# Kernel tuning notes

Measured on AMD Instinct MI355X. Metric: run time of the kernel, lower is better.

The kernel has to match this reference:

```python
import jax, jax.numpy as jnp
import numpy as np

N = 4096
IN_DIM, HID, OUT_DIM = 512, 256, 64
PROP_STEP = 10
LAM_HAT = 0.9
SCAD_A = 3.7
EPS = 1e-8


def setup_inputs() -> dict:
    key = jax.random.key(0)
    kA, kF, k1, k2 = jax.random.split(key, 4)
    # sparse symmetric 0/1 adjacency, zero diagonal (add_loops adds I later)
    u = jax.random.uniform(kA, (N, N), dtype=jnp.float32)
    A = (u < 0.005).astype(jnp.float32)
    A = jnp.maximum(A, A.T)
    A = A * (1.0 - jnp.eye(N, dtype=jnp.float32))
    F = jax.random.normal(kF, (N, IN_DIM), dtype=jnp.float32)
    W1 = jax.random.normal(k1, (IN_DIM, HID), dtype=jnp.float32) / np.sqrt(IN_DIM)
    b1 = jnp.zeros((HID,), dtype=jnp.float32)
    W2 = jax.random.normal(k2, (HID, OUT_DIM), dtype=jnp.float32) / np.sqrt(HID)
    b2 = jnp.zeros((OUT_DIM,), dtype=jnp.float32)
    raw_gamma = jnp.zeros((PROP_STEP,), dtype=jnp.float32)
    return {"A": A, "F": F, "W1": W1, "b1": b1, "W2": W2, "b2": b2,
            "raw_gamma": raw_gamma}


def reference(A, F, W1, b1, W2, b2, raw_gamma):
    lam = 1.0 / LAM_HAT - 1.0
    a = SCAD_A
    # MLP (dropout inactive at inference)
    F0 = jax.nn.relu(F @ W1 + b1) @ W2 + b2            # [N, out_dim]
    eye = jnp.eye(A.shape[0], dtype=A.dtype)
    A = A + eye                                        # add_loops
    D = A.sum(-1)                                      # [N]
    D_sq = jnp.sqrt(D)[:, None]                        # [N, 1]
    A_tilde = A / D_sq / D_sq.T                        # sym_norm: D^-1/2 A D^-1/2
    gammas = jax.nn.sigmoid(raw_gamma) * 2.0           # per-layer gamma in (0, 2)

    def step(Fc, gamma_k):
        Fn = Fc / D_sq
        nrm = jnp.linalg.norm(Fn, axis=-1, keepdims=True)
        Fu = Fn / jnp.maximum(nrm, 1e-12)
        # cosine distance in [0, 2]; detached as in torch (.detach())
        y = jax.lax.stop_gradient(1.0 - Fu @ Fu.T)     # [N, N]
        lam_k = jnp.maximum(gamma_k / a, EPS)
        t = a * lam_k
        safe_y = jnp.where(y <= 0.0, 1.0, y)
        w_mid = (t - y) / ((a - 1.0) * safe_y)
        # SCAD weight: 1 for y<=lam_k, linear decay on [lam_k, a*lam_k], 0 beyond
        W = jnp.where(y <= lam_k, 1.0, jnp.where(y <= t, w_mid, 0.0))
        W = W * (1.0 - eye)
        W = jnp.where(jnp.isnan(W), 1.0, W)
        Q_hat = ((W * A).sum(-1) / D + lam)[:, None]   # [N, 1]
        F_new = (W * A_tilde) @ Fc / Q_hat + lam * F0 / Q_hat
        return F_new, None

    F_out, _ = jax.lax.scan(step, F0, gammas)
    return F_out
```

## Files before the change

kernel.cpp:

```cpp
#include <hip/hip_runtime.h>
#include <hip/hip_bf16.h>

#define N_NODES 4096
#define IN_DIM  512
#define HID_DIM 256
#define OUT_DIM 64
#define PROP_STEP 10
#define MAX_DEG 128
#define GEMM_BLOCKS 256
#define SCAN_BLOCKS 256
#define LAM_CONST (1.0f/0.9f - 1.0f)
#define SCAD_A 3.7f

__device__ __forceinline__ ushort f2bf(float f) {
    unsigned u = __float_as_uint(f);
    unsigned r = (u + 0x7FFFu + ((u >> 16) & 1u)) >> 16;
    return (ushort)r;
}
__device__ __forceinline__ unsigned pack2(float lo, float hi) {
    return (unsigned)f2bf(lo) | ((unsigned)f2bf(hi) << 16);
}
__device__ __forceinline__ float bflo(unsigned u) { return __uint_as_float(u << 16); }
__device__ __forceinline__ float bfhi(unsigned u) { return __uint_as_float(u & 0xFFFF0000u); }

__global__ __launch_bounds__(512) void build_all(
    const float* __restrict__ A, const float* __restrict__ F,
    const float* __restrict__ W1, const float* __restrict__ b1,
    const float* __restrict__ W2, const float* __restrict__ b2,
    float* __restrict__ F0,
    int* __restrict__ ell, int* __restrict__ deg,
    float* __restrict__ invD, float* __restrict__ invDsq)
{
    if (blockIdx.x < GEMM_BLOCKS) {
        __shared__ float sFt[16][20];
        __shared__ float sW[16][272];
        __shared__ float sH[16][260];
        int t  = threadIdx.x;
        int m0 = blockIdx.x * 16;
        int tm = (t & 7) * 2;
        int tn = (t >> 3) * 4;
        int fr = t >> 4, fk = t & 15;
        int wr = t >> 6, wc = (t & 63) * 4;
        float a00 = 0.f, a01 = 0.f, a02 = 0.f, a03 = 0.f;
        float a10 = 0.f, a11 = 0.f, a12 = 0.f, a13 = 0.f;
        for (int kc = 0; kc < IN_DIM; kc += 16) {
            float fv = 0.0f;
            if (t < 256) fv = F[(size_t)(m0 + fr) * IN_DIM + kc + fk];
            float4 w0 = *(const float4*)(W1 + (size_t)(kc + wr)     * HID_DIM + wc);
            float4 w1 = *(const float4*)(W1 + (size_t)(kc + 8 + wr) * HID_DIM + wc);
            __syncthreads();
            if (t < 256) sFt[fk][fr] = fv;
            *(float4*)&sW[wr][wc]     = w0;
            *(float4*)&sW[8 + wr][wc] = w1;
            __syncthreads();
#pragma unroll
            for (int k = 0; k < 16; k++) {
                float2 a = *(const float2*)&sFt[k][tm];
                float4 b = *(const float4*)&sW[k][tn];
                a00 += a.x * b.x; a01 += a.x * b.y; a02 += a.x * b.z; a03 += a.x * b.w;
                a10 += a.y * b.x; a11 += a.y * b.y; a12 += a.y * b.z; a13 += a.y * b.w;
            }
        }
        float4 bb = *(const float4*)(b1 + tn);
        *(float4*)&sH[tm][tn] = make_float4(
            fmaxf(a00 + bb.x, 0.f), fmaxf(a01 + bb.y, 0.f),
            fmaxf(a02 + bb.z, 0.f), fmaxf(a03 + bb.w, 0.f));
        *(float4*)&sH[tm + 1][tn] = make_float4(
            fmaxf(a10 + bb.x, 0.f), fmaxf(a11 + bb.y, 0.f),
            fmaxf(a12 + bb.z, 0.f), fmaxf(a13 + bb.w, 0.f));
        __syncthreads();
        int r2 = t >> 5;
        int c2 = (t & 31) * 2;
        float accA = b2[c2], accB = b2[c2 + 1];
        float (*sW2c)[68] = (float(*)[68])sW;
        for (int kc = 0; kc < HID_DIM; kc += 64) {
            __syncthreads();
            for (int i = t; i < 1024; i += 512) {
                int kk = i >> 4, cc = (i & 15) * 4;
                *(float4*)&sW2c[kk][cc] =
                    *(const float4*)(W2 + (size_t)(kc + kk) * OUT_DIM + cc);
            }
            __syncthreads();
#pragma unroll 8
            for (int k = 0; k < 64; k++) {
                float  hb = sH[r2][kc + k];
                float2 w2 = *(const float2*)&sW2c[k][c2];
                accA += hb * w2.x; accB += hb * w2.y;
            }
        }
        *(float2*)(F0 + (size_t)(m0 + r2) * OUT_DIM + c2) = make_float2(accA, accB);
    } else {
        int sb   = blockIdx.x - GEMM_BLOCKS;
        int lane = threadIdx.x & 63;
        int wid  = threadIdx.x >> 6;
        int w    = sb * 8 + wid;
        for (int rr = 0; rr < 2; rr++) {
            int row = w * 2 + rr;
            const float* Arow = A + (size_t)row * N_NODES;
            float4 ch[16];
#pragma unroll
            for (int c = 0; c < 16; c++)
                ch[c] = *(const float4*)(Arow + c * 256 + lane * 4);
            int* rdst = ell + (size_t)row * MAX_DEG;
            unsigned cnt = 0;
#pragma unroll
            for (int c = 0; c < 16; c++) {
                float4 v = ch[c];
                int colbase = c * 256 + lane * 4;
#pragma unroll
                for (int q = 0; q < 4; q++) {
                    float vv = (q == 0) ? v.x : (q == 1) ? v.y : (q == 2) ? v.z : v.w;
                    bool nz = (vv != 0.0f);
                    unsigned long long m = __ballot(nz);
                    unsigned rank = __builtin_amdgcn_mbcnt_hi(
                        (unsigned)(m >> 32),
                        __builtin_amdgcn_mbcnt_lo((unsigned)m, 0u));
                    unsigned pos = cnt + rank;
                    if (nz && pos < MAX_DEG) rdst[pos] = colbase + q;
                    cnt += (unsigned)__popcll(m);
                }
            }
            int c  = (cnt > MAX_DEG) ? MAX_DEG : (int)cnt;
            int pad = (c + 15) & ~15;
            if (pad > MAX_DEG) pad = MAX_DEG;
            if (lane >= c && lane < pad) rdst[lane] = row;
            int l2 = lane + 64;
            if (l2 >= c && l2 < pad) rdst[l2] = row;
            if (lane == 0) {
                deg[row] = c;
                float d = (float)(cnt + 1);
                invD[row] = 1.0f / d;
                invDsq[row] = rsqrtf(d);
            }
        }
    }
}

__global__ __launch_bounds__(256, 4) void propagate_f0(
    const float* __restrict__ F0,
    const int* __restrict__ ell, const int* __restrict__ deg,
    const float* __restrict__ invD, const float* __restrict__ invDsq,
    const float* __restrict__ raw_gamma,
    unsigned* __restrict__ Pout, float* __restrict__ nrmOut)
{
    int lane = threadIdx.x & 63;
    int wid  = threadIdx.x >> 6;
    int r    = __builtin_amdgcn_readfirstlane(blockIdx.x * 4 + wid);
    int g    = lane >> 3;
    int sl   = lane & 7;
    const float inv_am1 = 1.0f / (SCAD_A - 1.0f);

    float gamma = 2.0f / (1.0f + expf(-raw_gamma[0]));
    float lam_k = fmaxf(gamma / SCAD_A, 1e-8f);
    float tt    = SCAD_A * lam_k;

    int dg = deg[r];
    int pad = (dg + 15) & ~15;
    int npair = pad >> 4;
    const int* nb = ell + (size_t)r * MAX_DEG;
    int ed0 = (lane < pad)      ? nb[lane]      : r;
    int ed1 = (64 + lane < pad) ? nb[64 + lane] : r;

    float iDs = invDsq[r];
    const float4* f04 = (const float4*)(F0 + (size_t)r * OUT_DIM + sl * 8);
    float4 fa = f04[0], fb = f04[1];
    float f0v[8] = { fa.x, fa.y, fa.z, fa.w, fb.x, fb.y, fb.z, fb.w };
    float ui[8];
    float ssr = 0.0f;
#pragma unroll
    for (int q = 0; q < 8; q++) { ui[q] = f0v[q] * iDs; ssr += ui[q] * ui[q]; }
    ssr += __shfl_xor(ssr, 1, 64);
    ssr += __shfl_xor(ssr, 2, 64);
    ssr += __shfl_xor(ssr, 4, 64);
    float inv_nr = 1.0f / fmaxf(sqrtf(ssr), 1e-12f);
#pragma unroll
    for (int q = 0; q < 8; q++) ui[q] *= inv_nr;

    float acc[8] = {};
    float qsum = 0.0f;
    for (int it = 0; it < npair; ++it) {
        int e0 = it * 16 + g, e1 = e0 + 8;
        int src = (it < 4) ? ed0 : ed1;
        int j0 = __shfl(src, e0 & 63, 64);
        int j1 = __shfl(src, e1 & 63, 64);
        const float4* p0 = (const float4*)(F0 + (size_t)j0 * OUT_DIM + sl * 8);
        const float4* p1 = (const float4*)(F0 + (size_t)j1 * OUT_DIM + sl * 8);
        float4 x0 = p0[0], x1 = p0[1];
        float4 y0 = p1[0], y1 = p1[1];
        float d0 = invDsq[j0], d1 = invDsq[j1];
        float v0[8] = { x0.x*d0, x0.y*d0, x0.z*d0, x0.w*d0, x1.x*d0, x1.y*d0, x1.z*d0, x1.w*d0 };
        float v1[8] = { y0.x*d1, y0.y*d1, y0.z*d1, y0.w*d1, y1.x*d1, y1.y*d1, y1.z*d1, y1.w*d1 };
        float pa = 0.f, pb = 0.f, s0 = 0.f, s1 = 0.f;
#pragma unroll
        for (int q = 0; q < 8; q++) {
            pa += ui[q] * v0[q]; s0 += v0[q] * v0[q];
            pb += ui[q] * v1[q]; s1 += v1[q] * v1[q];
        }
        pa += __shfl_xor(pa, 1, 64); pb += __shfl_xor(pb, 1, 64);
        s0 += __shfl_xor(s0, 1, 64); s1 += __shfl_xor(s1, 1, 64);
        pa += __shfl_xor(pa, 2, 64); pb += __shfl_xor(pb, 2, 64);
        s0 += __shfl_xor(s0, 2, 64); s1 += __shfl_xor(s1, 2, 64);
        pa += __shfl_xor(pa, 4, 64); pb += __shfl_xor(pb, 4, 64);
        s0 += __shfl_xor(s0, 4, 64); s1 += __shfl_xor(s1, 4, 64);
        float n0 = fmaxf(sqrtf(s0), 1e-12f);
        float n1 = fmaxf(sqrtf(s1), 1e-12f);
        float ya = 1.0f - pa / n0, yb = 1.0f - pb / n1;
        float wa = (ya <= lam_k) ? 1.0f : ((ya <= tt) ? (tt - ya) * inv_am1 / ya : 0.0f);
        float wb = (yb <= lam_k) ? 1.0f : ((yb <= tt) ? (tt - yb) * inv_am1 / yb : 0.0f);
        if (e0 >= dg) wa = 0.0f;
        if (e1 >= dg) wb = 0.0f;
        qsum += wa + wb;
#pragma unroll
        for (int q = 0; q < 8; q++) acc[q] += wa * v0[q] + wb * v1[q];
    }

#pragma unroll
    for (int off = 8; off <= 32; off <<= 1) {
#pragma unroll
        for (int q = 0; q < 8; q++) acc[q] += __shfl_xor(acc[q], off, 64);
        qsum += __shfl_xor(qsum, off, 64);
    }

    float Qh  = qsum * invD[r] + LAM_CONST;
    float rQh = 1.0f / Qh;
    float res[8], fn[8];
    float ssq = 0.0f;
#pragma unroll
    for (int q = 0; q < 8; q++) {
        res[q] = (acc[q] * iDs + LAM_CONST * f0v[q]) * rQh;
        fn[q]  = res[q] * iDs;
        ssq   += fn[q] * fn[q];
    }
    ssq += __shfl_xor(ssq, 1, 64);
    ssq += __shfl_xor(ssq, 2, 64);
    ssq += __shfl_xor(ssq, 4, 64);
    float nrm = fmaxf(sqrtf(ssq), 1e-12f);
    float inv_n = 1.0f / nrm;
    if (lane < 8) {
        uint4 fuPk;
        fuPk.x = pack2(fn[0] * inv_n, fn[1] * inv_n);
        fuPk.y = pack2(fn[2] * inv_n, fn[3] * inv_n);
        fuPk.z = pack2(fn[4] * inv_n, fn[5] * inv_n);
        fuPk.w = pack2(fn[6] * inv_n, fn[7] * inv_n);
        *(uint4*)(Pout + (size_t)r * 32 + sl * 4) = fuPk;
    }
    if (lane == 0) nrmOut[r] = nrm;
}

__global__ __launch_bounds__(256, 4) void propagate(
    const unsigned* __restrict__ Pin, const float* __restrict__ nrmIn,
    const float* __restrict__ F0,
    const int* __restrict__ ell, const int* __restrict__ deg,
    const float* __restrict__ invD, const float* __restrict__ invDsq,
    const float* __restrict__ raw_gamma, int step,
    unsigned* __restrict__ Pout, float* __restrict__ nrmOut,
    float* __restrict__ FcOut, int writeNext, int writeOut)
{
    int lane = threadIdx.x & 63;
    int wid  = threadIdx.x >> 6;
    int r    = __builtin_amdgcn_readfirstlane(blockIdx.x * 4 + wid);
    int g    = lane >> 3;
    int sl   = lane & 7;
    const float inv_am1 = 1.0f / (SCAD_A - 1.0f);

    float gamma = 2.0f / (1.0f + expf(-raw_gamma[step]));
    float lam_k = fmaxf(gamma / SCAD_A, 1e-8f);
    float tt    = SCAD_A * lam_k;

    int dg = deg[r];
    int pad = (dg + 15) & ~15;
    int npair = pad >> 4;
    const int* nb = ell + (size_t)r * MAX_DEG;
    int ed0 = (lane < pad)      ? nb[lane]      : r;
    int ed1 = (64 + lane < pad) ? nb[64 + lane] : r;

    uint4 up = *(const uint4*)(Pin + (size_t)r * 32 + sl * 4);
    float ui[8] = { bflo(up.x), bfhi(up.x), bflo(up.y), bfhi(up.y),
                    bflo(up.z), bfhi(up.z), bflo(up.w), bfhi(up.w) };

    float acc[8] = {};
    float qsum = 0.0f;

    auto eidx = [&](int it_, int& J0, int& J1) {
        int e0_ = it_ * 16 + g;
        int src = (it_ < 4) ? ed0 : ed1;
        J0 = __shfl(src, e0_ & 63, 64);
        J1 = __shfl(src, (e0_ + 8) & 63, 64);
    };
    auto body = [&](int it_, uint4 U0, uint4 U1, float NR0, float NR1) {
        float pa = ui[0] * bflo(U0.x) + ui[1] * bfhi(U0.x) + ui[2] * bflo(U0.y) + ui[3] * bfhi(U0.y)
                 + ui[4] * bflo(U0.z) + ui[5] * bfhi(U0.z) + ui[6] * bflo(U0.w) + ui[7] * bfhi(U0.w);
        float pb = ui[0] * bflo(U1.x) + ui[1] * bfhi(U1.x) + ui[2] * bflo(U1.y) + ui[3] * bfhi(U1.y)
                 + ui[4] * bflo(U1.z) + ui[5] * bfhi(U1.z) + ui[6] * bflo(U1.w) + ui[7] * bfhi(U1.w);
        pa += __shfl_xor(pa, 1, 64); pb += __shfl_xor(pb, 1, 64);
        pa += __shfl_xor(pa, 2, 64); pb += __shfl_xor(pb, 2, 64);
        pa += __shfl_xor(pa, 4, 64); pb += __shfl_xor(pb, 4, 64);
        float ya = 1.0f - pa, yb = 1.0f - pb;
        float wa = (ya <= lam_k) ? 1.0f : ((ya <= tt) ? (tt - ya) * inv_am1 / ya : 0.0f);
        float wb = (yb <= lam_k) ? 1.0f : ((yb <= tt) ? (tt - yb) * inv_am1 / yb : 0.0f);
        int e0_ = it_ * 16 + g;
        if (e0_ >= dg)     wa = 0.0f;
        if (e0_ + 8 >= dg) wb = 0.0f;
        qsum += wa + wb;
        float wsa = wa * NR0;
        float wsb = wb * NR1;
        acc[0] += wsa * bflo(U0.x) + wsb * bflo(U1.x);
        acc[1] += wsa * bfhi(U0.x) + wsb * bfhi(U1.x);
        acc[2] += wsa * bflo(U0.y) + wsb * bflo(U1.y);
        acc[3] += wsa * bfhi(U0.y) + wsb * bfhi(U1.y);
        acc[4] += wsa * bflo(U0.z) + wsb * bflo(U1.z);
        acc[5] += wsa * bfhi(U0.z) + wsb * bfhi(U1.z);
        acc[6] += wsa * bflo(U0.w) + wsb * bflo(U1.w);
        acc[7] += wsa * bfhi(U0.w) + wsb * bfhi(U1.w);
    };

    if (npair > 0) {
        uint4 uA0, uA1, uB0, uB1;
        float nA0, nA1, nB0, nB1;
        int j0, j1;
        eidx(0, j0, j1);
        uA0 = *(const uint4*)(Pin + (size_t)j0 * 32 + sl * 4);
        uA1 = *(const uint4*)(Pin + (size_t)j1 * 32 + sl * 4);
        nA0 = nrmIn[j0]; nA1 = nrmIn[j1];
        int it = 0;
        while (true) {
            if (it + 1 < npair) {
                eidx(it + 1, j0, j1);
                uB0 = *(const uint4*)(Pin + (size_t)j0 * 32 + sl * 4);
                uB1 = *(const uint4*)(Pin + (size_t)j1 * 32 + sl * 4);
                nB0 = nrmIn[j0]; nB1 = nrmIn[j1];
            }
            body(it, uA0, uA1, nA0, nA1);
            ++it; if (it >= npair) break;
            if (it + 1 < npair) {
                eidx(it + 1, j0, j1);
                uA0 = *(const uint4*)(Pin + (size_t)j0 * 32 + sl * 4);
                uA1 = *(const uint4*)(Pin + (size_t)j1 * 32 + sl * 4);
                nA0 = nrmIn[j0]; nA1 = nrmIn[j1];
            }
            body(it, uB0, uB1, nB0, nB1);
            ++it; if (it >= npair) break;
        }
    }

#pragma unroll
    for (int off = 8; off <= 32; off <<= 1) {
#pragma unroll
        for (int q = 0; q < 8; q++) acc[q] += __shfl_xor(acc[q], off, 64);
        qsum += __shfl_xor(qsum, off, 64);
    }

    float iDs = invDsq[r];
    float Qh  = qsum * invD[r] + LAM_CONST;
    float rQh = 1.0f / Qh;
    const float4* f04 = (const float4*)(F0 + (size_t)r * OUT_DIM + sl * 8);
    float4 f0a = f04[0], f0b = f04[1];
    float f0v[8] = { f0a.x, f0a.y, f0a.z, f0a.w, f0b.x, f0b.y, f0b.z, f0b.w };
    float res[8];
#pragma unroll
    for (int q = 0; q < 8; q++) res[q] = (acc[q] * iDs + LAM_CONST * f0v[q]) * rQh;

    if (writeOut && lane < 8) {
        float4* o4 = (float4*)(FcOut + (size_t)r * OUT_DIM + sl * 8);
        o4[0] = make_float4(res[0], res[1], res[2], res[3]);
        o4[1] = make_float4(res[4], res[5], res[6], res[7]);
    }
    if (writeNext) {
        float fn[8];
        float ssq = 0.0f;
#pragma unroll
        for (int q = 0; q < 8; q++) { fn[q] = res[q] * iDs; ssq += fn[q] * fn[q]; }
        ssq += __shfl_xor(ssq, 1, 64);
        ssq += __shfl_xor(ssq, 2, 64);
        ssq += __shfl_xor(ssq, 4, 64);
        float nrm = fmaxf(sqrtf(ssq), 1e-12f);
        float inv_n = 1.0f / nrm;
        if (lane < 8) {
            uint4 fuPk;
            fuPk.x = pack2(fn[0] * inv_n, fn[1] * inv_n);
            fuPk.y = pack2(fn[2] * inv_n, fn[3] * inv_n);
            fuPk.z = pack2(fn[4] * inv_n, fn[5] * inv_n);
            fuPk.w = pack2(fn[6] * inv_n, fn[7] * inv_n);
            *(uint4*)(Pout + (size_t)r * 32 + sl * 4) = fuPk;
        }
        if (lane == 0) nrmOut[r] = nrm;
    }
}

extern "C" void kernel_launch(void* const* d_in, const int* in_sizes, int n_in,
                              void* d_out, int out_size, void* d_ws, size_t ws_size,
                              hipStream_t stream)
{
    const float* A  = (const float*)d_in[0];
    const float* F  = (const float*)d_in[1];
    const float* W1 = (const float*)d_in[2];
    const float* b1 = (const float*)d_in[3];
    const float* W2 = (const float*)d_in[4];
    const float* b2 = (const float*)d_in[5];
    const float* rg = (const float*)d_in[6];
    float* out = (float*)d_out;

    char* p = (char*)d_ws;
    float* F0     = (float*)p; p += (size_t)N_NODES * OUT_DIM * 4;
    unsigned* Pa  = (unsigned*)p; p += (size_t)N_NODES * 32 * 4;
    unsigned* Pb  = (unsigned*)p; p += (size_t)N_NODES * 32 * 4;
    float* nrmA   = (float*)p; p += (size_t)N_NODES * 4;
    float* nrmB   = (float*)p; p += (size_t)N_NODES * 4;
    float* invD   = (float*)p; p += (size_t)N_NODES * 4;
    float* invDsq = (float*)p; p += (size_t)N_NODES * 4;
    int*   deg    = (int*)p;   p += (size_t)N_NODES * 4;
    int*   ell    = (int*)p;   p += (size_t)N_NODES * MAX_DEG * 4;

    build_all<<<GEMM_BLOCKS + SCAN_BLOCKS, 512, 0, stream>>>(
        A, F, W1, b1, W2, b2, F0, ell, deg, invD, invDsq);

    propagate_f0<<<N_NODES / 4, 256, 0, stream>>>(
        F0, ell, deg, invD, invDsq, rg, Pa, nrmA);

    for (int k = 1; k < PROP_STEP; k++) {
        unsigned* Pin   = (k & 1) ? Pa : Pb;
        unsigned* Pout  = (k & 1) ? Pb : Pa;
        float* nIn      = (k & 1) ? nrmA : nrmB;
        float* nOut     = (k & 1) ? nrmB : nrmA;
        int last = (k == PROP_STEP - 1);
        propagate<<<N_NODES / 4, 256, 0, stream>>>(
            Pin, nIn, F0, ell, deg, invD, invDsq, rg, k,
            Pout, nOut, out, !last, last);
    }
}
```

Before: 218.2 us.

## Restructure MLP GEMM in build_all with register-tiled W1 streaming and split-K W2

The MLP part of build_all is rewritten. The full 16x512 F tile is staged once in shared memory, W1 is streamed directly from global memory into registers with double-buffered float4 loads, and each thread accumulates a 4x4 output tile. The second GEMM splits K across four waves and reduces the partial sums through shared memory. The block size drops from 512 to 256 threads with launch_bounds(256,2), and each scan warp now handles 4 adjacency rows instead of 2. The aim is to remove per-chunk syncthreads and increase reuse in the GEMM, at the cost of more registers and less parallelism in the adjacency scan.

```diff
diff --git a/kernel.cpp b/kernel.cpp
--- a/kernel.cpp
+++ b/kernel.cpp
@@ -22,8 +22,33 @@
 }
 __device__ __forceinline__ float bflo(unsigned u) { return __uint_as_float(u << 16); }
 __device__ __forceinline__ float bfhi(unsigned u) { return __uint_as_float(u & 0xFFFF0000u); }
-
-__global__ __launch_bounds__(512) void build_all(
+__device__ __forceinline__ float4 f4add(float4 a, float4 b) {
+    return make_float4(a.x + b.x, a.y + b.y, a.z + b.z, a.w + b.w);
+}
+
+#define FMA16(AV, WV) \
+    acc0.x = fmaf(AV.x, WV.x, acc0.x); acc0.y = fmaf(AV.x, WV.y, acc0.y); \
+    acc0.z = fmaf(AV.x, WV.z, acc0.z); acc0.w = fmaf(AV.x, WV.w, acc0.w); \
+    acc1.x = fmaf(AV.y, WV.x, acc1.x); acc1.y = fmaf(AV.y, WV.y, acc1.y); \
+    acc1.z = fmaf(AV.y, WV.z, acc1.z); acc1.w = fmaf(AV.y, WV.w, acc1.w); \
+    acc2.x = fmaf(AV.z, WV.x, acc2.x); acc2.y = fmaf(AV.z, WV.y, acc2.y); \
+    acc2.z = fmaf(AV.z, WV.z, acc2.z); acc2.w = fmaf(AV.z, WV.w, acc2.w); \
+    acc3.x = fmaf(AV.w, WV.x, acc3.x); acc3.y = fmaf(AV.w, WV.y, acc3.y); \
+    acc3.z = fmaf(AV.w, WV.z, acc3.z); acc3.w = fmaf(AV.w, WV.w, acc3.w);
+
+#define STEP(KK, WV) { float4 a_ = *(const float4*)&sF[(KK) * 20 + rg4]; FMA16(a_, WV); }
+
+#define P2ROW(HV, PV) \
+    PV.x = fmaf(HV.x, w0.x, PV.x); PV.y = fmaf(HV.x, w0.y, PV.y); \
+    PV.z = fmaf(HV.x, w0.z, PV.z); PV.w = fmaf(HV.x, w0.w, PV.w); \
+    PV.x = fmaf(HV.y, w1.x, PV.x); PV.y = fmaf(HV.y, w1.y, PV.y); \
+    PV.z = fmaf(HV.y, w1.z, PV.z); PV.w = fmaf(HV.y, w1.w, PV.w); \
+    PV.x = fmaf(HV.z, w2.x, PV.x); PV.y = fmaf(HV.z, w2.y, PV.y); \
+    PV.z = fmaf(HV.z, w2.z, PV.z); PV.w = fmaf(HV.z, w2.w, PV.w); \
+    PV.x = fmaf(HV.w, w3.x, PV.x); PV.y = fmaf(HV.w, w3.y, PV.y); \
+    PV.z = fmaf(HV.w, w3.z, PV.z); PV.w = fmaf(HV.w, w3.w, PV.w);
+
+__global__ __launch_bounds__(256, 2) void build_all(
     const float* __restrict__ A, const float* __restrict__ F,
     const float* __restrict__ W1, const float* __restrict__ b1,
     const float* __restrict__ W2, const float* __restrict__ b2,
@@ -31,71 +56,131 @@
     int* __restrict__ ell, int* __restrict__ deg,
     float* __restrict__ invD, float* __restrict__ invDsq)
 {
+    __shared__ float smem[15360];
     if (blockIdx.x < GEMM_BLOCKS) {
-        __shared__ float sFt[16][20];
-        __shared__ float sW[16][272];
-        __shared__ float sH[16][260];
+        float* sF = smem;
         int t  = threadIdx.x;
         int m0 = blockIdx.x * 16;
-        int tm = (t & 7) * 2;
-        int tn = (t >> 3) * 4;
-        int fr = t >> 4, fk = t & 15;
-        int wr = t >> 6, wc = (t & 63) * 4;
-        float a00 = 0.f, a01 = 0.f, a02 = 0.f, a03 = 0.f;
-        float a10 = 0.f, a11 = 0.f, a12 = 0.f, a13 = 0.f;
-        for (int kc = 0; kc < IN_DIM; kc += 16) {
-            float fv = 0.0f;
-            if (t < 256) fv = F[(size_t)(m0 + fr) * IN_DIM + kc + fk];
-            float4 w0 = *(const float4*)(W1 + (size_t)(kc + wr)     * HID_DIM + wc);
-            float4 w1 = *(const float4*)(W1 + (size_t)(kc + 8 + wr) * HID_DIM + wc);
+        {
+            int r = t & 15, kc = (t >> 4) * 32;
+            const float* src = F + (size_t)(m0 + r) * IN_DIM + kc;
+#pragma unroll
+            for (int j = 0; j < 8; j++) {
+                float4 v = *(const float4*)(src + j * 4);
+                sF[(kc + j * 4 + 0) * 20 + r] = v.x;
+                sF[(kc + j * 4 + 1) * 20 + r] = v.y;
+                sF[(kc + j * 4 + 2) * 20 + r] = v.z;
+                sF[(kc + j * 4 + 3) * 20 + r] = v.w;
+            }
+        }
+        __syncthreads();
+        int rg4 = (t >> 6) * 4;
+        int cg  = t & 63;
+        const float* Wp = W1 + cg * 4;
+        float4 acc0 = {0,0,0,0}, acc1 = {0,0,0,0}, acc2 = {0,0,0,0}, acc3 = {0,0,0,0};
+        float4 wa0 = *(const float4*)(Wp + 0 * HID_DIM);
+        float4 wa1 = *(const float4*)(Wp + 1 * HID_DIM);
+        float4 wa2 = *(const float4*)(Wp + 2 * HID_DIM);
+        float4 wa3 = *(const float4*)(Wp + 3 * HID_DIM);
+        float4 wb0 = *(const float4*)(Wp + 4 * HID_DIM);
+        float4 wb1 = *(const float4*)(Wp + 5 * HID_DIM);
+        float4 wb2 = *(const float4*)(Wp + 6 * HID_DIM);
+        float4 wb3 = *(const float4*)(Wp + 7 * HID_DIM);
+        for (int kb = 0; kb < IN_DIM; kb += 8) {
+            STEP(kb + 0, wa0) STEP(kb + 1, wa1) STEP(kb + 2, wa2) STEP(kb + 3, wa3)
+            if (kb + 8 < IN_DIM) {
+                const float* wn = Wp + (size_t)(kb + 8) * HID_DIM;
+                wa0 = *(const float4*)(wn);
+                wa1 = *(const float4*)(wn + HID_DIM);
+                wa2 = *(const float4*)(wn + 2 * HID_DIM);
+                wa3 = *(const float4*)(wn + 3 * HID_DIM);
+            }
+            STEP(kb + 4, wb0) STEP(kb + 5, wb1) STEP(kb + 6, wb2) STEP(kb + 7, wb3)
+            if (kb + 8 < IN_DIM) {
+                const float* wn = Wp + (size_t)(kb + 12) * HID_DIM;
+                wb0 = *(const float4*)(wn);
+                wb1 = *(const float4*)(wn + HID_DIM);
+                wb2 = *(const float4*)(wn + 2 * HID_DIM);
+                wb3 = *(const float4*)(wn + 3 * HID_DIM);
+            }
+        }
+        __syncthreads();
+        float* sH   = smem;
+        float* sW2  = smem + 4096;
+        float* sRed = smem + 12288;
+        {
+            float4 bv = *(const float4*)(b1 + cg * 4);
+            float4 h0 = make_float4(fmaxf(acc0.x + bv.x, 0.f), fmaxf(acc0.y + bv.y, 0.f),
+                                    fmaxf(acc0.z + bv.z, 0.f), fmaxf(acc0.w + bv.w, 0.f));
+            float4 h1 = make_float4(fmaxf(acc1.x + bv.x, 0.f), fmaxf(acc1.y + bv.y, 0.f),
+                                    fmaxf(acc1.z + bv.z, 0.f), fmaxf(acc1.w + bv.w, 0.f));
+            float4 h2 = make_float4(fmaxf(acc2.x + bv.x, 0.f), fmaxf(acc2.y + bv.y, 0.f),
+                                    fmaxf(acc2.z + bv.z, 0.f), fmaxf(acc2.w + bv.w, 0.f));
+            float4 h3 = make_float4(fmaxf(acc3.x + bv.x, 0.f), fmaxf(acc3.y + bv.y, 0.f),
+                                    fmaxf(acc3.z + bv.z, 0.f), fmaxf(acc3.w + bv.w, 0.f));
+            *(float4*)&sH[(rg4 + 0) * 256 + cg * 4] = h0;
+            *(float4*)&sH[(rg4 + 1) * 256 + cg * 4] = h1;
+            *(float4*)&sH[(rg4 + 2) * 256 + cg * 4] = h2;
+            *(float4*)&sH[(rg4 + 3) * 256 + cg * 4] = h3;
+        }
+        int lane = t & 63, wid = t >> 6;
+        int rgrp = lane >> 4;
+        int cg2  = lane & 15;
+        float4 p0 = {0,0,0,0}, p1 = {0,0,0,0}, p2 = {0,0,0,0}, p3 = {0,0,0,0};
+        for (int hf = 0; hf < 2; hf++) {
+#pragma unroll
+            for (int i = 0; i < 8; i++) {
+                int flat = t + i * 256;
+                int kk = flat >> 4, c4 = (flat & 15) * 4;
+                *(float4*)&sW2[kk * 64 + c4] =
+                    *(const float4*)(W2 + (size_t)(hf * 128 + kk) * OUT_DIM + c4);
+            }
             __syncthreads();
-            if (t < 256) sFt[fk][fr] = fv;
-            *(float4*)&sW[wr][wc]     = w0;
-            *(float4*)&sW[8 + wr][wc] = w1;
+            int kbase = wid * 32;
+            for (int kq = 0; kq < 32; kq += 4) {
+                int kk = kbase + kq;
+                int kg = hf * 128 + kk;
+                float4 h0 = *(const float4*)&sH[(rgrp * 4 + 0) * 256 + kg];
+                float4 h1 = *(const float4*)&sH[(rgrp * 4 + 1) * 256 + kg];
+                float4 h2 = *(const float4*)&sH[(rgrp * 4 + 2) * 256 + kg];
+                float4 h3 = *(const float4*)&sH[(rgrp * 4 + 3) * 256 + kg];
+                float4 w0 = *(const float4*)&sW2[(kk + 0) * 64 + cg2 * 4];
+                float4 w1 = *(const float4*)&sW2[(kk + 1) * 64 + cg2 * 4];
+                float4 w2 = *(const float4*)&sW2[(kk + 2) * 64 + cg2 * 4];
+                float4 w3 = *(const float4*)&sW2[(kk + 3) * 64 + cg2 * 4];
+                P2ROW(h0, p0) P2ROW(h1, p1) P2ROW(h2, p2) P2ROW(h3, p3)
+            }
             __syncthreads();
-#pragma unroll
-            for (int k = 0; k < 16; k++) {
-                float2 a = *(const float2*)&sFt[k][tm];
-                float4 b = *(const float4*)&sW[k][tn];
-                a00 += a.x * b.x; a01 += a.x * b.y; a02 += a.x * b.z; a03 += a.x * b.w;
-                a10 += a.y * b.x; a11 += a.y * b.y; a12 += a.y * b.z; a13 += a.y * b.w;
-            }
-        }
-        float4 bb = *(const float4*)(b1 + tn);
-        *(float4*)&sH[tm][tn] = make_float4(
-            fmaxf(a00 + bb.x, 0.f), fmaxf(a01 + bb.y, 0.f),
-            fmaxf(a02 + bb.z, 0.f), fmaxf(a03 + bb.w, 0.f));
-        *(float4*)&sH[tm + 1][tn] = make_float4(
-            fmaxf(a10 + bb.x, 0.f), fmaxf(a11 + bb.y, 0.f),
-            fmaxf(a12 + bb.z, 0.f), fmaxf(a13 + bb.w, 0.f));
+        }
+        if (wid) {
+            float* dst = sRed + (size_t)(wid - 1) * 1024 + lane * 16;
+            *(float4*)(dst + 0)  = p0; *(float4*)(dst + 4)  = p1;
+            *(float4*)(dst + 8)  = p2; *(float4*)(dst + 12) = p3;
+        }
         __syncthreads();
-        int r2 = t >> 5;
-        int c2 = (t & 31) * 2;
-        float accA = b2[c2], accB = b2[c2 + 1];
-        float (*sW2c)[68] = (float(*)[68])sW;
-        for (int kc = 0; kc < HID_DIM; kc += 64) {
-            __syncthreads();
-            for (int i = t; i < 1024; i += 512) {
-                int kk = i >> 4, cc = (i & 15) * 4;
-                *(float4*)&sW2c[kk][cc] =
-                    *(const float4*)(W2 + (size_t)(kc + kk) * OUT_DIM + cc);
-            }
-            __syncthreads();
-#pragma unroll 8
-            for (int k = 0; k < 64; k++) {
-                float  hb = sH[r2][kc + k];
-                float2 w2 = *(const float2*)&sW2c[k][c2];
-                accA += hb * w2.x; accB += hb * w2.y;
-            }
-        }
-        *(float2*)(F0 + (size_t)(m0 + r2) * OUT_DIM + c2) = make_float2(accA, accB);
+        if (wid == 0) {
+#pragma unroll
+            for (int w = 0; w < 3; w++) {
+                const float* s = sRed + (size_t)w * 1024 + lane * 16;
+                p0 = f4add(p0, *(const float4*)(s + 0));
+                p1 = f4add(p1, *(const float4*)(s + 4));
+                p2 = f4add(p2, *(const float4*)(s + 8));
+                p3 = f4add(p3, *(const float4*)(s + 12));
+            }
+            float4 b2v = *(const float4*)(b2 + cg2 * 4);
+            float* o = F0 + (size_t)(m0 + rgrp * 4) * OUT_DIM + cg2 * 4;
+            *(float4*)(o + 0 * OUT_DIM) = f4add(p0, b2v);
+            *(float4*)(o + 1 * OUT_DIM) = f4add(p1, b2v);
+            *(float4*)(o + 2 * OUT_DIM) = f4add(p2, b2v);
+            *(float4*)(o + 3 * OUT_DIM) = f4add(p3, b2v);
+        }
     } else {
         int sb   = blockIdx.x - GEMM_BLOCKS;
         int lane = threadIdx.x & 63;
         int wid  = threadIdx.x >> 6;
-        int w    = sb * 8 + wid;
-        for (int rr = 0; rr < 2; rr++) {
-            int row = w * 2 + rr;
+        int w    = sb * 4 + wid;
+        for (int rr = 0; rr < 4; rr++) {
+            int row = w * 4 + rr;
             const float* Arow = A + (size_t)row * N_NODES;
             float4 ch[16];
 #pragma unroll
@@ -411,7 +496,7 @@
     int*   deg    = (int*)p;   p += (size_t)N_NODES * 4;
     int*   ell    = (int*)p;   p += (size_t)N_NODES * MAX_DEG * 4;
 
-    build_all<<<GEMM_BLOCKS + SCAN_BLOCKS, 512, 0, stream>>>(
+    build_all<<<GEMM_BLOCKS + SCAN_BLOCKS, 256, 0, stream>>>(
         A, F, W1, b1, W2, b2, F0, ell, deg, invD, invDsq);
 
     propagate_f0<<<N_NODES / 4, 256, 0, stream>>>(
```

Result: faster. 208.0 us (-4.7%).
